# Performance work log

Measured on AMD Instinct MI355X. Metric: run time of the kernel, lower is better.

Reference implementation:

```python
import jax, jax.numpy as jnp
import numpy as np

K = 10  # knn_graph default neighbors (self excluded)
NEG = 0.2  # LeakyReLU slope


def lrelu(x):
    return jnp.where(x > 0, x, NEG * x)


def conv1x1_1d(x, w):  # x: (B,Ci,N), w: (Co,Ci)
    return jnp.einsum('oi,bin->bon', w, x)


def conv1x1_2d(x, w):  # x: (B,Ci,N,k), w: (Co,Ci)
    return jnp.einsum('oi,bink->bonk', w, x)


def bn1(x, s, b):  # folded eval-mode BN, x: (B,C,N)
    return x * s[None, :, None] + b[None, :, None]


def bn2(x, s, b):  # x: (B,C,N,k)
    return x * s[None, :, None, None] + b[None, :, None, None]


def knn_graph(x, k=K):
    # x: (B, D, N) -> edge features (B, 2D, N, k)
    xt = jnp.transpose(x, (0, 2, 1))  # (B,N,D)
    sq = jnp.sum(xt * xt, axis=-1)  # (B,N)
    d2 = sq[:, :, None] + sq[:, None, :] - 2.0 * jnp.einsum('bnd,bmd->bnm', xt, xt)
    _, idx = jax.lax.top_k(-d2, k + 1)  # nearest k+1 incl. self
    idx = idx[:, :, 1:]  # drop self -> (B,N,k)
    B = xt.shape[0]
    feats = xt[jnp.arange(B)[:, None, None], idx]  # (B,N,k,D)
    center = xt[:, :, None, :]  # (B,N,1,D)
    edge = jnp.concatenate((feats - center, jnp.broadcast_to(center, feats.shape)), axis=-1)
    return jnp.transpose(edge, (0, 3, 1, 2))  # (B,2D,N,k)


def _make_params(key):
    ks = iter(jax.random.split(key, 32))
    def W(co, ci):
        return jax.random.normal(next(ks), (co, ci), jnp.float32) * (1.0 / np.sqrt(ci))
    def SB(c):
        return (jax.random.uniform(next(ks), (c,), jnp.float32, 0.5, 1.5),
                jax.random.normal(next(ks), (c,), jnp.float32) * 0.1)
    p = {}
    p['w1'] = W(64, 6);    p['s1'], p['b1'] = SB(64)
    p['w2'] = W(64, 64);   p['s2'], p['b2'] = SB(64)
    p['w3'] = W(64, 128);  p['s3'], p['b3'] = SB(64)
    p['w4'] = W(64, 64);   p['s4'], p['b4'] = SB(64)
    p['w5'] = W(64, 128);  p['s5'], p['b5'] = SB(64)
    p['w6'] = W(1024, 192); p['s6'], p['b6'] = SB(1024)
    p['w7'] = W(64, 16);   p['s7'], p['b7'] = SB(64)
    p['wp1'] = W(256, 1280); p['sp1'], p['bp1'] = SB(256)
    p['wp2'] = W(256, 256);  p['sp2'], p['bp2'] = SB(256)
    p['wp3'] = W(128, 256);  p['sp3'], p['bp3'] = SB(128)
    p['wp4'] = W(6, 128)
    return p


def setup_inputs() -> dict:
    key = jax.random.key(0)
    k0, k1, k2 = jax.random.split(key, 3)
    inp = {
        'points': jax.random.normal(k0, (8, 2048, 3), jnp.float32),
        'label': jax.random.uniform(k1, (8, 16), jnp.float32),
    }
    inp.update(_make_params(k2))
    return inp


def reference(points, label,
              w1, s1, b1, w2, s2, b2, w3, s3, b3, w4, s4, b4, w5, s5, b5,
              w6, s6, b6, w7, s7, b7,
              wp1, sp1, bp1, wp2, sp2, bp2, wp3, sp3, bp3, wp4):
    B, N, _ = points.shape
    x0 = jnp.transpose(points, (0, 2, 1))  # (B,3,N)

    e1 = knn_graph(x0)                                   # (B,6,N,k)
    h = lrelu(bn2(conv1x1_2d(e1, w1), s1, b1))
    out1 = jnp.max(lrelu(bn2(conv1x1_2d(h, w2), s2, b2)), axis=-1)  # (B,64,N)

    e2 = knn_graph(out1)                                 # (B,128,N,k)
    h = lrelu(bn2(conv1x1_2d(e2, w3), s3, b3))
    out2 = jnp.max(lrelu(bn2(conv1x1_2d(h, w4), s4, b4)), axis=-1)  # (B,64,N)

    e3 = knn_graph(out2)                                 # (B,128,N,k)
    out3 = jnp.max(lrelu(bn2(conv1x1_2d(e3, w5), s5, b5)), axis=-1)  # (B,64,N)

    comb = jnp.concatenate((out1, out2, out3), axis=1)   # (B,192,N)
    out4 = lrelu(bn1(conv1x1_1d(comb, w6), s6, b6))      # (B,1024,N)
    out4 = jnp.max(out4, axis=-1, keepdims=True)         # (B,1024,1)

    cat_vet = lrelu(bn1(conv1x1_1d(label[:, :, None], w7), s7, b7))  # (B,64,1)
    glob = jnp.broadcast_to(jnp.concatenate((out4, cat_vet), axis=1), (B, 1088, N))

    out = jnp.concatenate((out1, out2, out3, glob), axis=1)  # (B,1280,N)
    out = lrelu(bn1(conv1x1_1d(out, wp1), sp1, bp1))
    out = lrelu(bn1(conv1x1_1d(out, wp2), sp2, bp2))  # dropout = identity (eval)
    out = lrelu(bn1(conv1x1_1d(out, wp3), sp3, bp3))
    out = conv1x1_1d(out, wp4)                         # (B,6,N)
    return jnp.transpose(out, (0, 2, 1))               # (B,N,6)
```

## Files before the change

### kernel.cpp

```cpp
#include <hip/hip_runtime.h>
#include <float.h>

#define NEG 0.2f
constexpr int BATCH = 8;
constexpr int NPTS  = 2048;
constexpr int KNN   = 10;
constexpr int KP1   = 11;

__device__ __forceinline__ float lrelu(float x) { return x > 0.f ? x : NEG * x; }

__device__ __forceinline__ unsigned long long dkey(float d, int m) {
    unsigned u = __float_as_uint(d);
    u ^= (unsigned)((int)u >> 31) | 0x80000000u;
    return ((unsigned long long)u << 32) | (unsigned)m;
}

template<int D>
__global__ void sq_kernel(const float* __restrict__ xt, float* __restrict__ sq) {
    int i = blockIdx.x * 256 + threadIdx.x;
    if (i >= BATCH * NPTS) return;
    const float* p = xt + (size_t)i * D;
    float s = 0.f;
    #pragma unroll
    for (int d = 0; d < D; ++d) s += p[d] * p[d];
    sq[i] = s;
}

__global__ void sq64_kernel(const float* __restrict__ xt, float* __restrict__ sq) {
    int i = blockIdx.x * 256 + threadIdx.x;
    if (i >= BATCH * NPTS) return;
    const float4* p = (const float4*)(xt + (size_t)i * 64);
    float4 s4 = {0.f, 0.f, 0.f, 0.f};
    #pragma unroll
    for (int d = 0; d < 16; ++d) {
        float4 v = p[d];
        s4.x += v.x * v.x; s4.y += v.y * v.y; s4.z += v.z * v.z; s4.w += v.w * v.w;
    }
    sq[i] = (s4.x + s4.y) + (s4.z + s4.w);
}

__global__ __launch_bounds__(64) void knn3_kernel(const float* __restrict__ xt,
                                                  const float* __restrict__ sq,
                                                  int* __restrict__ idx_out) {
    const int bn = blockIdx.x;
    const int b  = bn >> 11;
    const int l  = threadIdx.x;

    const float qx = xt[(size_t)bn * 3 + 0];
    const float qy = xt[(size_t)bn * 3 + 1];
    const float qz = xt[(size_t)bn * 3 + 2];
    const float sqn = sq[bn];
    const float* xb  = xt + (size_t)b * NPTS * 3;
    const float* sqb_ = sq + (size_t)b * NPTS;

    unsigned long long lk[KP1];
    #pragma unroll
    for (int j = 0; j < KP1; ++j) lk[j] = ~0ULL;

    for (int m = l; m < NPTS; m += 64) {
        float dot = 0.f;
        dot += qx * xb[m * 3 + 0];
        dot += qy * xb[m * 3 + 1];
        dot += qz * xb[m * 3 + 2];
        float cd = sqn + sqb_[m] - 2.f * dot;
        unsigned long long key = dkey(cd, m);
        if (key < lk[KP1 - 1]) {
            #pragma unroll
            for (int j = 0; j < KP1; ++j) {
                bool better = key < lk[j];
                unsigned long long tk = lk[j];
                if (better) { lk[j] = key; key = tk; }
            }
        }
    }

    #pragma unroll
    for (int k = 0; k < KP1; ++k) {
        unsigned long long mk = lk[0];
        #pragma unroll
        for (int s = 32; s >= 1; s >>= 1) {
            unsigned long long o = __shfl_xor(mk, s, 64);
            mk = (o < mk) ? o : mk;
        }
        if (k >= 1 && l == k - 1)
            idx_out[(size_t)bn * KNN + (k - 1)] = (int)(unsigned)mk;
        if (lk[0] == mk) {
            #pragma unroll
            for (int j = 0; j < KP1 - 1; ++j) lk[j] = lk[j + 1];
            lk[KP1 - 1] = ~0ULL;
        }
    }
}

__global__ __launch_bounds__(256) void knn64_kernel(const float* __restrict__ xt,
                                                    const float* __restrict__ sq,
                                                    int* __restrict__ idx_out) {
    const int t  = threadIdx.x;
    const int qg = t >> 5;
    const int lc = t & 31;
    const int bn0 = blockIdx.x * 8;
    const int bn  = bn0 + qg;
    const int b   = bn >> 11;
    const float* xb = xt + (size_t)b * NPTS * 64;

    __shared__ __align__(16) float4 tile4[32][16];

    float4 xq[16];
    {
        const float4* xqp = (const float4*)(xt + (size_t)bn * 64);
        #pragma unroll
        for (int i = 0; i < 16; ++i) xq[i] = xqp[i];
    }
    const float sqn = sq[bn];
    const float* sqb_ = sq + b * NPTS;

    unsigned long long lk[KP1];
    #pragma unroll
    for (int j = 0; j < KP1; ++j) lk[j] = ~0ULL;

    const int ci  = t >> 3;
    const int sub = t & 7;

    for (int t0 = 0; t0 < NPTS; t0 += 32) {
        __syncthreads();
        {
            const float4* src = (const float4*)(xb + (size_t)(t0 + ci) * 64 + sub * 8);
            float4 u0 = src[0], u1 = src[1];
            tile4[ci][(2 * sub)     ^ (ci & 15)] = u0;
            tile4[ci][(2 * sub + 1) ^ (ci & 15)] = u1;
        }
        __syncthreads();

        const int m = t0 + lc;
        float a0 = 0.f, a1 = 0.f, a2 = 0.f, a3 = 0.f;
        #pragma unroll
        for (int i = 0; i < 16; ++i) {
            float4 v = tile4[lc][i ^ (lc & 15)];
            a0 += xq[i].x * v.x;
            a1 += xq[i].y * v.y;
            a2 += xq[i].z * v.z;
            a3 += xq[i].w * v.w;
        }
        float dot = (a0 + a1) + (a2 + a3);
        float cd = sqn + sqb_[m] - 2.f * dot;
        unsigned long long key = dkey(cd, m);
        if (key < lk[KP1 - 1]) {
            #pragma unroll
            for (int j = 0; j < KP1; ++j) {
                bool better = key < lk[j];
                unsigned long long tk = lk[j];
                if (better) { lk[j] = key; key = tk; }
            }
        }
    }

    #pragma unroll
    for (int k = 0; k < KP1; ++k) {
        unsigned long long mk = lk[0];
        #pragma unroll
        for (int s = 16; s >= 1; s >>= 1) {
            unsigned long long o = __shfl_xor(mk, s, 32);
            mk = (o < mk) ? o : mk;
        }
        if (k >= 1 && lc == k - 1)
            idx_out[(size_t)bn * KNN + (k - 1)] = (int)(unsigned)mk;
        if (lk[0] == mk) {
            #pragma unroll
            for (int j = 0; j < KP1 - 1; ++j) lk[j] = lk[j + 1];
            lk[KP1 - 1] = ~0ULL;
        }
    }
}

__global__ __launch_bounds__(64) void edgeconv1_kernel(
    const float* __restrict__ pts, const int* __restrict__ idx,
    const float* __restrict__ w1, const float* __restrict__ s1, const float* __restrict__ b1,
    const float* __restrict__ w2, const float* __restrict__ s2, const float* __restrict__ b2,
    float* __restrict__ outt) {
    const int bn = blockIdx.x;
    const int b  = bn / NPTS;
    const int c  = threadIdx.x;

    const float cx = pts[bn * 3 + 0], cy = pts[bn * 3 + 1], cz = pts[bn * 3 + 2];

    float w1r[6];
    #pragma unroll
    for (int i = 0; i < 6; ++i) w1r[i] = w1[c * 6 + i];
    const float s1c = s1[c], b1c = b1[c], s2c = s2[c], b2c = b2[c];

    __shared__ float h1all[KNN][64];
    #pragma unroll
    for (int k = 0; k < KNN; ++k) {
        const int m = idx[bn * KNN + k];
        const float* f = pts + ((size_t)b * NPTS + m) * 3;
        const float e0 = f[0] - cx, e1 = f[1] - cy, e2 = f[2] - cz;
        float a = w1r[0] * e0 + w1r[1] * e1 + w1r[2] * e2
                + w1r[3] * cx + w1r[4] * cy + w1r[5] * cz;
        h1all[k][c] = lrelu(a * s1c + b1c);
    }
    __syncthreads();

    float a2[KNN];
    #pragma unroll
    for (int k = 0; k < KNN; ++k) a2[k] = 0.f;
    for (int j4 = 0; j4 < 16; ++j4) {
        float4 wv = *(const float4*)&w2[c * 64 + j4 * 4];
        #pragma unroll
        for (int k = 0; k < KNN; ++k) {
            float4 h4 = *(const float4*)&h1all[k][j4 * 4];
            a2[k] += wv.x * h4.x + wv.y * h4.y + wv.z * h4.z + wv.w * h4.w;
        }
    }
    float mx = -FLT_MAX;
    #pragma unroll
    for (int k = 0; k < KNN; ++k) mx = fmaxf(mx, lrelu(a2[k] * s2c + b2c));
    outt[(size_t)bn * 64 + c] = mx;
}

__global__ __launch_bounds__(64) void edgeconv2_kernel(
    const float* __restrict__ xin, const int* __restrict__ idx,
    const float* __restrict__ w3, const float* __restrict__ s3, const float* __restrict__ b3,
    const float* __restrict__ w4, const float* __restrict__ s4, const float* __restrict__ b4,
    float* __restrict__ outt) {
    const int bn = blockIdx.x;
    const int b  = bn / NPTS;
    const int c  = threadIdx.x;

    __shared__ float cen[64];
    __shared__ float fea[KNN][64];
    __shared__ float h1all[KNN][64];
    cen[c] = xin[(size_t)bn * 64 + c];
    #pragma unroll
    for (int k = 0; k < KNN; ++k) {
        const int m = idx[bn * KNN + k];
        fea[k][c] = xin[((size_t)b * NPTS + m) * 64 + c];
    }
    __syncthreads();

    float a[KNN];
    #pragma unroll
    for (int k = 0; k < KNN; ++k) a[k] = 0.f;
    float4 ab = {0.f, 0.f, 0.f, 0.f};
    for (int j4 = 0; j4 < 16; ++j4) {
        float4 wa = *(const float4*)&w3[c * 128 + j4 * 4];
        float4 wb = *(const float4*)&w3[c * 128 + 64 + j4 * 4];
        float4 c4 = *(const float4*)&cen[j4 * 4];
        ab.x += (wb.x - wa.x) * c4.x; ab.y += (wb.y - wa.y) * c4.y;
        ab.z += (wb.z - wa.z) * c4.z; ab.w += (wb.w - wa.w) * c4.w;
        #pragma unroll
        for (int k = 0; k < KNN; ++k) {
            float4 f4 = *(const float4*)&fea[k][j4 * 4];
            a[k] += wa.x * f4.x + wa.y * f4.y + wa.z * f4.z + wa.w * f4.w;
        }
    }
    const float abase = (ab.x + ab.y) + (ab.z + ab.w);
    const float s3c = s3[c], b3c = b3[c], s4c = s4[c], b4c = b4[c];
    #pragma unroll
    for (int k = 0; k < KNN; ++k) h1all[k][c] = lrelu((a[k] + abase) * s3c + b3c);
    __syncthreads();

    float a2[KNN];
    #pragma unroll
    for (int k = 0; k < KNN; ++k) a2[k] = 0.f;
    for (int j4 = 0; j4 < 16; ++j4) {
        float4 wv = *(const float4*)&w4[c * 64 + j4 * 4];
        #pragma unroll
        for (int k = 0; k < KNN; ++k) {
            float4 h4 = *(const float4*)&h1all[k][j4 * 4];
            a2[k] += wv.x * h4.x + wv.y * h4.y + wv.z * h4.z + wv.w * h4.w;
        }
    }
    float mx = -FLT_MAX;
    #pragma unroll
    for (int k = 0; k < KNN; ++k) mx = fmaxf(mx, lrelu(a2[k] * s4c + b4c));
    outt[(size_t)bn * 64 + c] = mx;
}

__global__ __launch_bounds__(64) void edgeconv3_kernel(
    const float* __restrict__ xin, const int* __restrict__ idx,
    const float* __restrict__ w5, const float* __restrict__ s5, const float* __restrict__ b5,
    float* __restrict__ outt) {
    const int bn = blockIdx.x;
    const int b  = bn / NPTS;
    const int c  = threadIdx.x;

    __shared__ float cen[64];
    __shared__ float fea[KNN][64];
    cen[c] = xin[(size_t)bn * 64 + c];
    #pragma unroll
    for (int k = 0; k < KNN; ++k) {
        const int m = idx[bn * KNN + k];
        fea[k][c] = xin[((size_t)b * NPTS + m) * 64 + c];
    }
    __syncthreads();

    float a[KNN];
    #pragma unroll
    for (int k = 0; k < KNN; ++k) a[k] = 0.f;
    float4 ab = {0.f, 0.f, 0.f, 0.f};
    for (int j4 = 0; j4 < 16; ++j4) {
        float4 wa = *(const float4*)&w5[c * 128 + j4 * 4];
        float4 wb = *(const float4*)&w5[c * 128 + 64 + j4 * 4];
        float4 c4 = *(const float4*)&cen[j4 * 4];
        ab.x += (wb.x - wa.x) * c4.x; ab.y += (wb.y - wa.y) * c4.y;
        ab.z += (wb.z - wa.z) * c4.z; ab.w += (wb.w - wa.w) * c4.w;
        #pragma unroll
        for (int k = 0; k < KNN; ++k) {
            float4 f4 = *(const float4*)&fea[k][j4 * 4];
            a[k] += wa.x * f4.x + wa.y * f4.y + wa.z * f4.z + wa.w * f4.w;
        }
    }
    const float abase = (ab.x + ab.y) + (ab.z + ab.w);
    const float s5c = s5[c], b5c = b5[c];
    float mx = -FLT_MAX;
    #pragma unroll
    for (int k = 0; k < KNN; ++k) mx = fmaxf(mx, lrelu((a[k] + abase) * s5c + b5c));
    outt[(size_t)bn * 64 + c] = mx;
}

__global__ __launch_bounds__(64) void catvet_kernel(
    const float* __restrict__ label,
    const float* __restrict__ w7, const float* __restrict__ s7, const float* __restrict__ b7,
    float* __restrict__ catv) {
    const int b = blockIdx.x, c = threadIdx.x;
    float a = 0.f;
    #pragma unroll
    for (int i = 0; i < 16; ++i) a += w7[c * 16 + i] * label[b * 16 + i];
    catv[b * 64 + c] = lrelu(a * s7[c] + b7[c]);
}

__global__ void w6t_kernel(const float* __restrict__ w6, float* __restrict__ w6t) {
    int i = blockIdx.x * 256 + threadIdx.x;
    if (i >= 192 * 1024) return;
    int k = i >> 10, c = i & 1023;
    w6t[i] = w6[c * 192 + k];
}

constexpr int OPTS = 32;
__global__ __launch_bounds__(256) void out4max_kernel(
    const float* __restrict__ out1t, const float* __restrict__ out2t, const float* __restrict__ out3t,
    const float* __restrict__ w6t, float* __restrict__ partial) {
    const int blk = blockIdx.x;
    const int b   = blk >> 6;
    const int nt  = blk & 63;
    const int t   = threadIdx.x;

    __shared__ float xs[192 * OPTS];
    for (int idx = t; idx < 192 * OPTS; idx += 256) {
        int p = idx / 192, r = idx - p * 192;
        const size_t gp = (size_t)b * NPTS + nt * OPTS + p;
        float val;
        if (r < 64)       val = out1t[gp * 64 + r];
        else if (r < 128) val = out2t[gp * 64 + (r - 64)];
        else              val = out3t[gp * 64 + (r - 128)];
        xs[r * OPTS + p] = val;
    }
    __syncthreads();

    float mx0 = -FLT_MAX, mx1 = -FLT_MAX, mx2 = -FLT_MAX, mx3 = -FLT_MAX;
    #pragma unroll
    for (int pg = 0; pg < OPTS / 16; ++pg) {
        float acc0[16], acc1[16], acc2[16], acc3[16];
        #pragma unroll
        for (int p = 0; p < 16; ++p) { acc0[p] = 0.f; acc1[p] = 0.f; acc2[p] = 0.f; acc3[p] = 0.f; }
        #pragma unroll 2
        for (int k = 0; k < 192; ++k) {
            float4 wv = *(const float4*)&w6t[(size_t)k * 1024 + t * 4];
            const float4* xr4 = (const float4*)&xs[k * OPTS + pg * 16];
            #pragma unroll
            for (int p4 = 0; p4 < 4; ++p4) {
                float4 xv = xr4[p4];
                acc0[p4 * 4 + 0] += wv.x * xv.x; acc0[p4 * 4 + 1] += wv.x * xv.y;
                acc0[p4 * 4 + 2] += wv.x * xv.z; acc0[p4 * 4 + 3] += wv.x * xv.w;
                acc1[p4 * 4 + 0] += wv.y * xv.x; acc1[p4 * 4 + 1] += wv.y * xv.y;
                acc1[p4 * 4 + 2] += wv.y * xv.z; acc1[p4 * 4 + 3] += wv.y * xv.w;
                acc2[p4 * 4 + 0] += wv.z * xv.x; acc2[p4 * 4 + 1] += wv.z * xv.y;
                acc2[p4 * 4 + 2] += wv.z * xv.z; acc2[p4 * 4 + 3] += wv.z * xv.w;
                acc3[p4 * 4 + 0] += wv.w * xv.x; acc3[p4 * 4 + 1] += wv.w * xv.y;
                acc3[p4 * 4 + 2] += wv.w * xv.z; acc3[p4 * 4 + 3] += wv.w * xv.w;
            }
        }
        #pragma unroll
        for (int p = 0; p < 16; ++p) {
            mx0 = fmaxf(mx0, acc0[p]); mx1 = fmaxf(mx1, acc1[p]);
            mx2 = fmaxf(mx2, acc2[p]); mx3 = fmaxf(mx3, acc3[p]);
        }
    }
    float4 o = {mx0, mx1, mx2, mx3};
    *(float4*)&partial[(size_t)blk * 1024 + t * 4] = o;
}

__global__ __launch_bounds__(256) void out4reduce_kernel(
    const float* __restrict__ partial,
    const float* __restrict__ s6, const float* __restrict__ b6,
    float* __restrict__ out4m) {
    const int i = blockIdx.x * 256 + threadIdx.x;
    const int b = i >> 10, c = i & 1023;
    float m = -FLT_MAX;
    for (int nt = 0; nt < 64; ++nt)
        m = fmaxf(m, partial[((size_t)b * 64 + nt) * 1024 + c]);
    out4m[i] = lrelu(m * s6[c] + b6[c]);
}

__global__ __launch_bounds__(256) void gbias_kernel(
    const float* __restrict__ out4m, const float* __restrict__ catv,
    const float* __restrict__ wp1, float* __restrict__ g) {
    const int b = blockIdx.x, t = threadIdx.x;
    __shared__ float v[1088];
    for (int i = t; i < 1088; i += 256)
        v[i] = (i < 1024) ? out4m[(size_t)b * 1024 + i] : catv[(size_t)b * 64 + (i - 1024)];
    __syncthreads();
    const float* w = wp1 + (size_t)t * 1280 + 192;
    float4 s4 = {0.f, 0.f, 0.f, 0.f};
    for (int i = 0; i < 272; ++i) {
        float4 wv = *(const float4*)&w[i * 4];
        float4 vv = *(const float4*)&v[i * 4];
        s4.x += wv.x * vv.x; s4.y += wv.y * vv.y; s4.z += wv.z * vv.z; s4.w += wv.w * vv.w;
    }
    g[(size_t)b * 256 + t] = (s4.x + s4.y) + (s4.z + s4.w);
}

constexpr int HP = 16;
constexpr int KC = 16;

__global__ __launch_bounds__(256) void head_kernel(
    const float* __restrict__ out1t, const float* __restrict__ out2t, const float* __restrict__ out3t,
    const float* __restrict__ g,
    const float* __restrict__ wp1, const float* __restrict__ sp1, const float* __restrict__ bp1,
    const float* __restrict__ wp2, const float* __restrict__ sp2, const float* __restrict__ bp2,
    const float* __restrict__ wp3, const float* __restrict__ sp3, const float* __restrict__ bp3,
    const float* __restrict__ wp4, float* __restrict__ out) {
    const int p0 = blockIdx.x * HP;
    const int b  = p0 >> 11;
    const int t  = threadIdx.x;

    __shared__ float smA[4096];
    __shared__ float smB[4096];
    __shared__ float smW[KC * 256];

    for (int e = t; e < 192 * HP; e += 256) {
        int p = e / 192, k = e - p * 192;
        float val;
        if (k < 64)       val = out1t[((size_t)(p0 + p)) * 64 + k];
        else if (k < 128) val = out2t[((size_t)(p0 + p)) * 64 + (k - 64)];
        else              val = out3t[((size_t)(p0 + p)) * 64 + (k - 128)];
        smA[k * HP + p] = val;
    }

    const int og = t & 31;
    const int pg = t >> 5;

    float acc[2][8];
    #pragma unroll
    for (int i = 0; i < 8; ++i) {
        float gv = g[(size_t)b * 256 + og * 8 + i];
        acc[0][i] = gv; acc[1][i] = gv;
    }
    for (int kc = 0; kc < 192 / KC; ++kc) {
        __syncthreads();
        #pragma unroll
        for (int it = 0; it < KC; ++it)
            smW[it * 256 + t] = wp1[(size_t)t * 1280 + kc * KC + it];
        __syncthreads();
        #pragma unroll 4
        for (int kk = 0; kk < KC; ++kk) {
            int k = kc * KC + kk;
            float2 xv = *(const float2*)&smA[k * HP + pg * 2];
            float4 w0 = *(const float4*)&smW[kk * 256 + og * 8];
            float4 w1v = *(const float4*)&smW[kk * 256 + og * 8 + 4];
            float wv[8] = {w0.x, w0.y, w0.z, w0.w, w1v.x, w1v.y, w1v.z, w1v.w};
            #pragma unroll
            for (int i = 0; i < 8; ++i) {
                acc[0][i] += xv.x * wv[i];
                acc[1][i] += xv.y * wv[i];
            }
        }
    }
    #pragma unroll
    for (int i = 0; i < 8; ++i) {
        int o = og * 8 + i;
        float sc = sp1[o], bc = bp1[o];
        smB[o * HP + pg * 2 + 0] = lrelu(acc[0][i] * sc + bc);
        smB[o * HP + pg * 2 + 1] = lrelu(acc[1][i] * sc + bc);
    }

    float acc2[2][8];
    #pragma unroll
    for (int i = 0; i < 8; ++i) { acc2[0][i] = 0.f; acc2[1][i] = 0.f; }
    for (int kc = 0; kc < 256 / KC; ++kc) {
        __syncthreads();
        #pragma unroll
        for (int it = 0; it < KC; ++it)
            smW[it * 256 + t] = wp2[(size_t)t * 256 + kc * KC + it];
        __syncthreads();
        #pragma unroll 4
        for (int kk = 0; kk < KC; ++kk) {
            int k = kc * KC + kk;
            float2 xv = *(const float2*)&smB[k * HP + pg * 2];
            float4 w0 = *(const float4*)&smW[kk * 256 + og * 8];
            float4 w1v = *(const float4*)&smW[kk * 256 + og * 8 + 4];
            float wv[8] = {w0.x, w0.y, w0.z, w0.w, w1v.x, w1v.y, w1v.z, w1v.w};
            #pragma unroll
            for (int i = 0; i < 8; ++i) {
                acc2[0][i] += xv.x * wv[i];
                acc2[1][i] += xv.y * wv[i];
            }
        }
    }
    __syncthreads();
    #pragma unroll
    for (int i = 0; i < 8; ++i) {
        int o = og * 8 + i;
        float sc = sp2[o], bc = bp2[o];
        smA[o * HP + pg * 2 + 0] = lrelu(acc2[0][i] * sc + bc);
        smA[o * HP + pg * 2 + 1] = lrelu(acc2[1][i] * sc + bc);
    }

    const int og3 = t & 15;
    const int p3  = t >> 4;
    float acc3[8];
    #pragma unroll
    for (int i = 0; i < 8; ++i) acc3[i] = 0.f;
    for (int kc = 0; kc < 256 / KC; ++kc) {
        __syncthreads();
        for (int e = t; e < KC * 128; e += 256) {
            int kk = e >> 7, o = e & 127;
            smW[kk * 128 + o] = wp3[(size_t)o * 256 + kc * KC + kk];
        }
        __syncthreads();
        #pragma unroll 4
        for (int kk = 0; kk < KC; ++kk) {
            int k = kc * KC + kk;
            float xv = smA[k * HP + p3];
            float4 w0 = *(const float4*)&smW[kk * 128 + og3 * 8];
            float4 w1v = *(const float4*)&smW[kk * 128 + og3 * 8 + 4];
            float wv[8] = {w0.x, w0.y, w0.z, w0.w, w1v.x, w1v.y, w1v.z, w1v.w};
            #pragma unroll
            for (int i = 0; i < 8; ++i) acc3[i] += xv * wv[i];
        }
    }
    __syncthreads();
    #pragma unroll
    for (int i = 0; i < 8; ++i) {
        int o = og3 * 8 + i;
        float sc = sp3[o], bc = bp3[o];
        smB[o * HP + p3] = lrelu(acc3[i] * sc + bc);
    }
    __syncthreads();

    if (t < HP * 6) {
        int p = t / 6, o = t - p * 6;
        float4 s4 = {0.f, 0.f, 0.f, 0.f};
        for (int k4 = 0; k4 < 32; ++k4) {
            float4 wv = *(const float4*)&wp4[o * 128 + k4 * 4];
            s4.x += wv.x * smB[(k4 * 4 + 0) * HP + p];
            s4.y += wv.y * smB[(k4 * 4 + 1) * HP + p];
            s4.z += wv.z * smB[(k4 * 4 + 2) * HP + p];
            s4.w += wv.w * smB[(k4 * 4 + 3) * HP + p];
        }
        out[((size_t)(p0 + p)) * 6 + o] = (s4.x + s4.y) + (s4.z + s4.w);
    }
}

extern "C" void kernel_launch(void* const* d_in, const int* in_sizes, int n_in,
                              void* d_out, int out_size, void* d_ws, size_t ws_size,
                              hipStream_t stream) {
    const float* points = (const float*)d_in[0];
    const float* label  = (const float*)d_in[1];
    const float* w1  = (const float*)d_in[2];
    const float* s1  = (const float*)d_in[3];
    const float* b1  = (const float*)d_in[4];
    const float* w2  = (const float*)d_in[5];
    const float* s2  = (const float*)d_in[6];
    const float* b2  = (const float*)d_in[7];
    const float* w3  = (const float*)d_in[8];
    const float* s3  = (const float*)d_in[9];
    const float* b3  = (const float*)d_in[10];
    const float* w4  = (const float*)d_in[11];
    const float* s4  = (const float*)d_in[12];
    const float* b4  = (const float*)d_in[13];
    const float* w5  = (const float*)d_in[14];
    const float* s5  = (const float*)d_in[15];
    const float* b5  = (const float*)d_in[16];
    const float* w6  = (const float*)d_in[17];
    const float* s6  = (const float*)d_in[18];
    const float* b6  = (const float*)d_in[19];
    const float* w7  = (const float*)d_in[20];
    const float* s7  = (const float*)d_in[21];
    const float* b7  = (const float*)d_in[22];
    const float* wp1 = (const float*)d_in[23];
    const float* sp1 = (const float*)d_in[24];
    const float* bp1 = (const float*)d_in[25];
    const float* wp2 = (const float*)d_in[26];
    const float* sp2 = (const float*)d_in[27];
    const float* bp2 = (const float*)d_in[28];
    const float* wp3 = (const float*)d_in[29];
    const float* sp3 = (const float*)d_in[30];
    const float* bp3 = (const float*)d_in[31];
    const float* wp4 = (const float*)d_in[32];

    float* ws = (float*)d_ws;
    size_t off = 0;
    auto alloc = [&](size_t nf) { float* p = ws + off; off += nf; return p; };
    float* out1t = alloc((size_t)BATCH * NPTS * 64);
    float* out2t = alloc((size_t)BATCH * NPTS * 64);
    float* out3t = alloc((size_t)BATCH * NPTS * 64);
    float* sqb   = alloc((size_t)BATCH * NPTS);
    float* out4m = alloc((size_t)BATCH * 1024);
    float* catv  = alloc((size_t)BATCH * 64);
    float* gb    = alloc((size_t)BATCH * 256);
    float* w6t   = alloc((size_t)192 * 1024);
    float* part  = alloc((size_t)512 * 1024);
    int* idx1 = (int*)alloc((size_t)BATCH * NPTS * KNN);
    int* idx2 = (int*)alloc((size_t)BATCH * NPTS * KNN);
    int* idx3 = (int*)alloc((size_t)BATCH * NPTS * KNN);

    const int BN = BATCH * NPTS;
    const int sqBlocks = (BN + 255) / 256;

    sq_kernel<3><<<sqBlocks, 256, 0, stream>>>(points, sqb);
    knn3_kernel<<<BN, 64, 0, stream>>>(points, sqb, idx1);
    edgeconv1_kernel<<<BN, 64, 0, stream>>>(points, idx1, w1, s1, b1, w2, s2, b2, out1t);

    sq64_kernel<<<sqBlocks, 256, 0, stream>>>(out1t, sqb);
    knn64_kernel<<<BN / 8, 256, 0, stream>>>(out1t, sqb, idx2);
    edgeconv2_kernel<<<BN, 64, 0, stream>>>(out1t, idx2, w3, s3, b3, w4, s4, b4, out2t);

    sq64_kernel<<<sqBlocks, 256, 0, stream>>>(out2t, sqb);
    knn64_kernel<<<BN / 8, 256, 0, stream>>>(out2t, sqb, idx3);
    edgeconv3_kernel<<<BN, 64, 0, stream>>>(out2t, idx3, w5, s5, b5, out3t);

    catvet_kernel<<<BATCH, 64, 0, stream>>>(label, w7, s7, b7, catv);
    w6t_kernel<<<(192 * 1024 + 255) / 256, 256, 0, stream>>>(w6, w6t);
    out4max_kernel<<<512, 256, 0, stream>>>(out1t, out2t, out3t, w6t, part);
    out4reduce_kernel<<<BATCH * 1024 / 256, 256, 0, stream>>>(part, s6, b6, out4m);
    gbias_kernel<<<BATCH, 256, 0, stream>>>(out4m, catv, wp1, gb);

    head_kernel<<<BN / HP, 256, 0, stream>>>(out1t, out2t, out3t, gb,
                                             wp1, sp1, bp1, wp2, sp2, bp2, wp3, sp3, bp3,
                                             wp4, (float*)d_out);
}
```

Baseline: 1.116 ms.

## Double-buffer knn64 tiles and split dot products across half-wavefronts

The 64-dim kNN kernel now double-buffers the shared-memory candidate tile, prefetching the next tile into registers while the current one is processed. This drops one barrier per iteration and hides global load latency. Each half-wavefront now computes half of the dimensions for two queries and combines the partial sums with a cross-lane shuffle. That halves LDS reads per query, at the cost of extra shuffles and more register pressure.

```diff
diff --git a/kernel.cpp b/kernel.cpp
--- a/kernel.cpp
+++ b/kernel.cpp
@@ -98,18 +98,23 @@
     const int t  = threadIdx.x;
     const int qg = t >> 5;
     const int lc = t & 31;
+    const int h  = qg & 1;
+    const int w  = t >> 6;
     const int bn0 = blockIdx.x * 8;
     const int bn  = bn0 + qg;
+    const int qA  = bn0 + 2 * w;
+    const int qB  = qA + 1;
     const int b   = bn >> 11;
     const float* xb = xt + (size_t)b * NPTS * 64;
 
-    __shared__ __align__(16) float4 tile4[32][16];
-
-    float4 xq[16];
+    __shared__ __align__(16) float4 tile4[2][32][16];
+
+    float4 xqa[8], xqb[8];
     {
-        const float4* xqp = (const float4*)(xt + (size_t)bn * 64);
-        #pragma unroll
-        for (int i = 0; i < 16; ++i) xq[i] = xqp[i];
+        const float4* pa = (const float4*)(xt + (size_t)qA * 64 + h * 32);
+        const float4* pb = (const float4*)(xt + (size_t)qB * 64 + h * 32);
+        #pragma unroll
+        for (int i = 0; i < 8; ++i) { xqa[i] = pa[i]; xqb[i] = pb[i]; }
     }
     const float sqn = sq[bn];
     const float* sqb_ = sq + b * NPTS;
@@ -121,27 +126,40 @@
     const int ci  = t >> 3;
     const int sub = t & 7;
 
+    {
+        const float4* src = (const float4*)(xb + (size_t)ci * 64 + sub * 8);
+        float4 u0 = src[0], u1 = src[1];
+        tile4[0][ci][(2 * sub)     ^ (ci & 15)] = u0;
+        tile4[0][ci][(2 * sub + 1) ^ (ci & 15)] = u1;
+    }
+    __syncthreads();
+
+    int cur = 0;
     for (int t0 = 0; t0 < NPTS; t0 += 32) {
-        __syncthreads();
-        {
-            const float4* src = (const float4*)(xb + (size_t)(t0 + ci) * 64 + sub * 8);
-            float4 u0 = src[0], u1 = src[1];
-            tile4[ci][(2 * sub)     ^ (ci & 15)] = u0;
-            tile4[ci][(2 * sub + 1) ^ (ci & 15)] = u1;
-        }
-        __syncthreads();
+        float4 n0, n1;
+        const bool more = (t0 + 32 < NPTS);
+        if (more) {
+            const float4* src = (const float4*)(xb + (size_t)(t0 + 32 + ci) * 64 + sub * 8);
+            n0 = src[0]; n1 = src[1];
+        }
+
+        float a0 = 0.f, a1 = 0.f, a2 = 0.f, a3 = 0.f;
+        float c0 = 0.f, c1 = 0.f, c2 = 0.f, c3 = 0.f;
+        #pragma unroll
+        for (int i = 0; i < 8; ++i) {
+            float4 v = tile4[cur][lc][(h * 8 + i) ^ (lc & 15)];
+            a0 += xqa[i].x * v.x; a1 += xqa[i].y * v.y;
+            a2 += xqa[i].z * v.z; a3 += xqa[i].w * v.w;
+            c0 += xqb[i].x * v.x; c1 += xqb[i].y * v.y;
+            c2 += xqb[i].z * v.z; c3 += xqb[i].w * v.w;
+        }
+        float pA = (a0 + a1) + (a2 + a3);
+        float pB = (c0 + c1) + (c2 + c3);
+        float oA = __shfl_xor(pA, 32, 64);
+        float oB = __shfl_xor(pB, 32, 64);
+        float dot = (h == 0) ? (pA + oA) : (oB + pB);
 
         const int m = t0 + lc;
-        float a0 = 0.f, a1 = 0.f, a2 = 0.f, a3 = 0.f;
-        #pragma unroll
-        for (int i = 0; i < 16; ++i) {
-            float4 v = tile4[lc][i ^ (lc & 15)];
-            a0 += xq[i].x * v.x;
-            a1 += xq[i].y * v.y;
-            a2 += xq[i].z * v.z;
-            a3 += xq[i].w * v.w;
-        }
-        float dot = (a0 + a1) + (a2 + a3);
         float cd = sqn + sqb_[m] - 2.f * dot;
         unsigned long long key = dkey(cd, m);
         if (key < lk[KP1 - 1]) {
@@ -152,6 +170,13 @@
                 if (better) { lk[j] = key; key = tk; }
             }
         }
+
+        if (more) {
+            tile4[cur ^ 1][ci][(2 * sub)     ^ (ci & 15)] = n0;
+            tile4[cur ^ 1][ci][(2 * sub + 1) ^ (ci & 15)] = n1;
+        }
+        __syncthreads();
+        cur ^= 1;
     }
 
     #pragma unroll
```

New measurement: 1.082 ms. 3.1% less time.
